# Optimization experiments

Measured on AMD Instinct MI355X. Metric: run time of the kernel, lower is better.

The kernel has to match this reference:

```python
import jax, jax.numpy as jnp
import numpy as np

SIGMA_PRIOR = 0.5   # sigma init kwarg; logvar_prior = log(sigma), sigma_prior = exp(logvar_prior) = sigma
TEMP = 1.0
LN_EPS = 1e-5
DIM, NQ, NK = 256, 512, 512


def setup_inputs() -> dict:
    key = jax.random.key(0)
    ks = jax.random.split(key, 10)
    s = 1.0 / np.sqrt(DIM)
    return {
        "Q": jax.random.normal(ks[0], (NQ, DIM), jnp.float32),
        "K": jax.random.normal(ks[1], (NK, DIM), jnp.float32),
        "V": jax.random.normal(ks[2], (NK, DIM), jnp.float32),
        "eps": jax.random.normal(ks[3], (NQ, NK), jnp.float32),
        # prior MLP: Linear(dim,dim) -> ReLU -> Linear(dim,1)
        "W1p": jax.random.normal(ks[4], (DIM, DIM), jnp.float32) * s,
        "b1p": jnp.zeros((DIM,), jnp.float32),
        "w2p": jax.random.normal(ks[5], (DIM,), jnp.float32) * s,
        "b2p": jnp.zeros((), jnp.float32),
        # posterior MLP: Linear(2*dim, dim) -> ReLU
        "Wpost": jax.random.normal(ks[6], (DIM, 2 * DIM), jnp.float32) * s,
        "bpost": jnp.zeros((DIM,), jnp.float32),
        # mu / logvar heads: Linear(dim, 1)
        "w_mu": jax.random.normal(ks[7], (DIM,), jnp.float32) * s,
        "b_mu": jnp.zeros((), jnp.float32),
        "w_lv": jax.random.normal(ks[8], (DIM,), jnp.float32) * s,
        "b_lv": jnp.zeros((), jnp.float32),
        # output LayerNorm(dim)
        "gamma": jnp.ones((DIM,), jnp.float32),
        "beta": jnp.zeros((DIM,), jnp.float32),
    }


def reference(Q, K, V, eps, W1p, b1p, w2p, b2p, Wpost, bpost,
              w_mu, b_mu, w_lv, b_lv, gamma, beta):
    dim = Q.shape[-1]
    sigma_prior = jnp.float32(SIGMA_PRIOR)

    # --- prior: mlp_prior(K) per key; broadcast over queries (identical math to K_exp) ---
    h = jax.nn.relu(K @ W1p.T + b1p)                       # [Nk, dim]
    mu_prior = h @ w2p + b2p - 0.5 * sigma_prior ** 2      # [Nk]

    # --- posterior: Linear on cat([Q_exp, K_exp]) == Q@Wq^T + K@Wk^T + b ---
    Wq, Wk = Wpost[:, :dim], Wpost[:, dim:]
    latent = jax.nn.relu((Q @ Wq.T)[:, None, :] + (K @ Wk.T + bpost)[None, :, :])  # [Nq, Nk, dim]
    phi = latent @ w_mu + b_mu                             # [Nq, Nk]
    logvar = latent @ w_lv + b_lv                          # [Nq, Nk]
    sig = jnp.exp(0.5 * logvar)
    mu = phi - 0.5 * sig ** 2

    # --- KL(prior || posterior form used by the module) ---
    term0 = jnp.log(sigma_prior / sig)
    term1 = (sig ** 2 + (mu - mu_prior[None, :]) ** 2) / (2.0 * sigma_prior ** 2)
    kl = jnp.mean(term0 + term1 - 0.5)

    # --- reparameterized sample, softmax weights, context ---
    samples = jnp.exp(mu + sig * eps) / TEMP               # [Nq, Nk]
    weights = jax.nn.softmax(samples, axis=-1)
    context = weights @ V                                  # [Nq, dim]

    # --- LayerNorm(dim) ---
    m = jnp.mean(context, axis=-1, keepdims=True)
    v = jnp.var(context, axis=-1, keepdims=True)
    out = (context - m) / jnp.sqrt(v + LN_EPS) * gamma + beta
    return (out, kl)
```

## Files before the change

kernel.cpp:

```cpp
#include <hip/hip_runtime.h>
#include <hip/hip_fp16.h>
#include <math.h>

#define DIM 256
#define NQ  512
#define NK  512

#define WS_A   0
#define WS_B   (NQ*DIM)
#define WS_MP  (WS_B + NK*DIM)
#define WS_S   (WS_MP + 512)
#define WS_P   (WS_S + NQ*NK)
#define WS_VH  (WS_P + 256)

__global__ __launch_bounds__(512) void k1_precompute(
    const float* __restrict__ Q, const float* __restrict__ Km,
    const float* __restrict__ V,
    const float* __restrict__ W1p, const float* __restrict__ b1p,
    const float* __restrict__ w2p, const float* __restrict__ b2p,
    const float* __restrict__ Wpost, const float* __restrict__ bpost,
    float* __restrict__ A, float* __restrict__ B, float* __restrict__ mu_prior,
    __half2* __restrict__ Vh2)
{
    __shared__ float X_lds[4][DIM];
    __shared__ float red[2][4][260];
    const int tid = threadIdx.x;
    const int bid = blockIdx.x;
    const int job = bid >> 7;

    if (job == 3) {
        const int pb = (bid - 384) * 4096 + tid;
        #pragma unroll
        for (int j = 0; j < 8; ++j) {
            int p = pb + 512 * j;
            float2 f = ((const float2*)V)[p];
            Vh2[p] = __floats2half2_rn(f.x, f.y);
        }
        return;
    }

    const int r0  = (bid & 127) * 4;
    const float* X = (job == 0) ? Q : Km;
    const float* W = (job == 2) ? W1p : Wpost;
    const int wstride = (job == 2) ? DIM : 2 * DIM;
    const int wcol    = (job == 1) ? DIM : 0;

    if (tid < 256) {
        int row = tid >> 6, c4 = tid & 63;
        *(float4*)&X_lds[row][c4 * 4] = *(const float4*)&X[(r0 + row) * DIM + c4 * 4];
    }
    __syncthreads();

    const int c  = tid & 255;
    const int dh = tid >> 8;
    const float* wrow = W + c * wstride + wcol + dh * 128;
    const float* xrow0 = &X_lds[0][dh * 128];

    float acc0 = 0.f, acc1 = 0.f, acc2 = 0.f, acc3 = 0.f;
    #pragma unroll 8
    for (int d0 = 0; d0 < 128; d0 += 4) {
        float4 w4 = *(const float4*)&wrow[d0];
        float4 x0 = *(const float4*)&xrow0[d0];
        float4 x1 = *(const float4*)&xrow0[DIM + d0];
        float4 x2 = *(const float4*)&xrow0[2 * DIM + d0];
        float4 x3 = *(const float4*)&xrow0[3 * DIM + d0];
        acc0 = fmaf(x0.x, w4.x, acc0); acc0 = fmaf(x0.y, w4.y, acc0);
        acc0 = fmaf(x0.z, w4.z, acc0); acc0 = fmaf(x0.w, w4.w, acc0);
        acc1 = fmaf(x1.x, w4.x, acc1); acc1 = fmaf(x1.y, w4.y, acc1);
        acc1 = fmaf(x1.z, w4.z, acc1); acc1 = fmaf(x1.w, w4.w, acc1);
        acc2 = fmaf(x2.x, w4.x, acc2); acc2 = fmaf(x2.y, w4.y, acc2);
        acc2 = fmaf(x2.z, w4.z, acc2); acc2 = fmaf(x2.w, w4.w, acc2);
        acc3 = fmaf(x3.x, w4.x, acc3); acc3 = fmaf(x3.y, w4.y, acc3);
        acc3 = fmaf(x3.z, w4.z, acc3); acc3 = fmaf(x3.w, w4.w, acc3);
    }
    red[dh][0][c] = acc0; red[dh][1][c] = acc1;
    red[dh][2][c] = acc2; red[dh][3][c] = acc3;
    __syncthreads();

    if (job < 2) {
        if (tid < 256) {
            #pragma unroll
            for (int r = 0; r < 4; ++r) {
                float v = red[0][r][c] + red[1][r][c];
                if (job == 0) A[(r0 + r) * DIM + c] = v;
                else          B[(r0 + r) * DIM + c] = v + bpost[c];
            }
        }
    } else {
        if (tid < 256) {
            float b1 = b1p[c], w2 = w2p[c];
            #pragma unroll
            for (int r = 0; r < 4; ++r)
                red[0][r][c] = fmaxf(red[0][r][c] + red[1][r][c] + b1, 0.f) * w2;
        }
        __syncthreads();
        int w = tid >> 6, lane = tid & 63;
        if (w < 4) {
            float v = red[0][w][lane] + red[0][w][lane + 64]
                    + red[0][w][lane + 128] + red[0][w][lane + 192];
            #pragma unroll
            for (int off = 32; off; off >>= 1) v += __shfl_xor(v, off);
            if (lane == 0) mu_prior[r0 + w] = v + b2p[0] - 0.125f;
        }
    }
}

__global__ __launch_bounds__(512) void k2_latent(
    const float* __restrict__ A, const float* __restrict__ B,
    const float* __restrict__ mu_prior, const float* __restrict__ eps,
    const float* __restrict__ w_mu, const float* __restrict__ b_mu,
    const float* __restrict__ w_lv, const float* __restrict__ b_lv,
    float* __restrict__ samples, float* __restrict__ partials)
{
    __shared__ float A_lds[32][260];
    __shared__ float B_lds[32][260];
    __shared__ float wm[DIM], wl[DIM];
    __shared__ float red[2][256][9];
    __shared__ float wred[8];
    const int tid = threadIdx.x;
    const int bq0 = (blockIdx.x >> 4) * 32;
    const int bk0 = (blockIdx.x & 15) * 32;

    #pragma unroll
    for (int i = 0; i < 4; ++i) {
        int f4 = tid + 512 * i;
        int row = f4 >> 6, c4 = f4 & 63;
        *(float4*)&A_lds[row][c4 * 4] = *(const float4*)&A[(bq0 + row) * DIM + c4 * 4];
        *(float4*)&B_lds[row][c4 * 4] = *(const float4*)&B[(bk0 + row) * DIM + c4 * 4];
    }
    if (tid < 256) { wm[tid] = w_mu[tid]; wl[tid] = w_lv[tid]; }
    __syncthreads();

    const int l  = tid & 255;
    const int dh = tid >> 8;
    const int tq = l >> 4, tk = l & 15;
    const int db = dh * 128;

    float p00 = 0, p01 = 0, p10 = 0, p11 = 0;
    float l00 = 0, l01 = 0, l10 = 0, l11 = 0;

    #pragma unroll 4
    for (int dd = 0; dd < 128; dd += 4) {
        int d0 = db + dd;
        float4 a0 = *(const float4*)&A_lds[tq][d0];
        float4 a1 = *(const float4*)&A_lds[tq + 16][d0];
        float4 b0 = *(const float4*)&B_lds[tk][d0];
        float4 b1 = *(const float4*)&B_lds[tk + 16][d0];
        float4 m4 = *(const float4*)&wm[d0];
        float4 v4 = *(const float4*)&wl[d0];
#define STEP(c) { float r_;                                                      \
        r_ = fmaxf(a0.c + b0.c, 0.f); p00 = fmaf(r_, m4.c, p00); l00 = fmaf(r_, v4.c, l00); \
        r_ = fmaxf(a0.c + b1.c, 0.f); p01 = fmaf(r_, m4.c, p01); l01 = fmaf(r_, v4.c, l01); \
        r_ = fmaxf(a1.c + b0.c, 0.f); p10 = fmaf(r_, m4.c, p10); l10 = fmaf(r_, v4.c, l10); \
        r_ = fmaxf(a1.c + b1.c, 0.f); p11 = fmaf(r_, m4.c, p11); l11 = fmaf(r_, v4.c, l11); }
        STEP(x) STEP(y) STEP(z) STEP(w)
#undef STEP
    }

    red[dh][l][0] = p00; red[dh][l][1] = l00;
    red[dh][l][2] = p01; red[dh][l][3] = l01;
    red[dh][l][4] = p10; red[dh][l][5] = l10;
    red[dh][l][6] = p11; red[dh][l][7] = l11;
    __syncthreads();

    float kls = 0.f;
    {
        const float bmu = b_mu[0], blv = b_lv[0];
        const int l2 = tid & 255;
        const int ih = tid >> 8;
        const int tq2 = l2 >> 4, tk2 = l2 & 15;
        const int q_  = bq0 + tq2 + 16 * ih;
        const int ka_ = bk0 + tk2, kb_ = ka_ + 16;
        const float mpa = mu_prior[ka_], mpb = mu_prior[kb_];
        const float C0 = -0.69314718056f - 0.5f;

#define FINISH(i, k, mp) {                                          \
        float pacc = red[0][l2][2*(i)]   + red[1][l2][2*(i)];       \
        float lacc = red[0][l2][2*(i)+1] + red[1][l2][2*(i)+1];     \
        float lv   = lacc + blv;                                    \
        float phi  = pacc + bmu;                                    \
        float sig  = __expf(0.5f * lv);                             \
        float sig2 = sig * sig;                                     \
        float mu   = phi - 0.5f * sig2;                             \
        float dm   = mu - (mp);                                     \
        kls += C0 - 0.5f * lv + 2.f * (sig2 + dm * dm);             \
        samples[q_ * NK + (k)] = __expf(mu + sig * eps[q_ * NK + (k)]); }

        FINISH(2 * ih,     ka_, mpa)
        FINISH(2 * ih + 1, kb_, mpb)
#undef FINISH
    }

    #pragma unroll
    for (int off = 32; off; off >>= 1) kls += __shfl_xor(kls, off);
    if ((tid & 63) == 0) wred[tid >> 6] = kls;
    __syncthreads();
    if (tid == 0) {
        float s = 0.f;
        #pragma unroll
        for (int i = 0; i < 8; ++i) s += wred[i];
        partials[blockIdx.x] = s;
    }
}

__global__ __launch_bounds__(512) void k3_output(
    const float* __restrict__ samples, const __half2* __restrict__ Vh2,
    const float* __restrict__ gamma, const float* __restrict__ beta,
    const float* __restrict__ partials, float* __restrict__ out)
{
    __shared__ float w_lds[2][NK];
    __shared__ float redbuf[16][DIM];
    __shared__ float sred[8][2], ssum[8][2], klr[8], lnred[8][2];
    const int tid = threadIdx.x;
    const int q0 = blockIdx.x * 2;
    const int wv = tid >> 6, lane = tid & 63;

    if (blockIdx.x == 0) {
        float v = (tid < 256) ? partials[tid] : 0.f;
        #pragma unroll
        for (int off = 32; off; off >>= 1) v += __shfl_xor(v, off);
        if (lane == 0) klr[wv] = v;
        __syncthreads();
        if (tid == 0) {
            float s = 0.f;
            #pragma unroll
            for (int i = 0; i < 8; ++i) s += klr[i];
            out[NQ * DIM] = s * (1.f / (float)(NQ * NK));
        }
    }

    float s0 = samples[q0 * NK + tid];
    float s1 = samples[(q0 + 1) * NK + tid];
    float m0 = s0, m1 = s1;
    #pragma unroll
    for (int off = 32; off; off >>= 1) {
        m0 = fmaxf(m0, __shfl_xor(m0, off));
        m1 = fmaxf(m1, __shfl_xor(m1, off));
    }
    if (lane == 0) { sred[wv][0] = m0; sred[wv][1] = m1; }
    __syncthreads();
    m0 = sred[0][0]; m1 = sred[0][1];
    #pragma unroll
    for (int i = 1; i < 8; ++i) {
        m0 = fmaxf(m0, sred[i][0]);
        m1 = fmaxf(m1, sred[i][1]);
    }
    float e0 = __expf(s0 - m0), e1 = __expf(s1 - m1);
    w_lds[0][tid] = e0;
    w_lds[1][tid] = e1;
    float t0 = e0, t1 = e1;
    #pragma unroll
    for (int off = 32; off; off >>= 1) {
        t0 += __shfl_xor(t0, off);
        t1 += __shfl_xor(t1, off);
    }
    if (lane == 0) { ssum[wv][0] = t0; ssum[wv][1] = t1; }
    __syncthreads();
    float sum0 = 0.f, sum1 = 0.f;
    #pragma unroll
    for (int i = 0; i < 8; ++i) { sum0 += ssum[i][0]; sum1 += ssum[i][1]; }
    const float inv0 = 1.f / sum0, inv1 = 1.f / sum1;

    const int g = tid & 63, s = tid >> 6;
    float a00 = 0, a01 = 0, a02 = 0, a03 = 0;
    float a10 = 0, a11 = 0, a12 = 0, a13 = 0;
    const __half2* vp = Vh2 + s * 64 * (DIM / 2) + 2 * g;
    #pragma unroll 8
    for (int i = 0; i < 64; ++i) {
        float2 raw = *(const float2*)(vp + i * (DIM / 2));
        __half2 h0 = *(__half2*)&raw.x;
        __half2 h1 = *(__half2*)&raw.y;
        float2 f0 = __half22float2(h0);
        float2 f1 = __half22float2(h1);
        int k = s * 64 + i;
        float w0 = w_lds[0][k], w1 = w_lds[1][k];
        a00 = fmaf(w0, f0.x, a00); a01 = fmaf(w0, f0.y, a01);
        a02 = fmaf(w0, f1.x, a02); a03 = fmaf(w0, f1.y, a03);
        a10 = fmaf(w1, f0.x, a10); a11 = fmaf(w1, f0.y, a11);
        a12 = fmaf(w1, f1.x, a12); a13 = fmaf(w1, f1.y, a13);
    }
    *(float4*)&redbuf[s * 2 + 0][4 * g] = make_float4(a00, a01, a02, a03);
    *(float4*)&redbuf[s * 2 + 1][4 * g] = make_float4(a10, a11, a12, a13);
    __syncthreads();

    const int r = tid >> 8, col = tid & 255;
    float c = 0.f;
    #pragma unroll
    for (int j = 0; j < 8; ++j) c += redbuf[j * 2 + r][col];
    c *= (r == 0) ? inv0 : inv1;
    float s1v = c, s2v = c * c;
    #pragma unroll
    for (int off = 32; off; off >>= 1) {
        s1v += __shfl_xor(s1v, off);
        s2v += __shfl_xor(s2v, off);
    }
    if (lane == 0) { lnred[wv][0] = s1v; lnred[wv][1] = s2v; }
    __syncthreads();
    float mean = (lnred[4 * r][0] + lnred[4 * r + 1][0] + lnred[4 * r + 2][0] + lnred[4 * r + 3][0]) * (1.f / DIM);
    float msq  = (lnred[4 * r][1] + lnred[4 * r + 1][1] + lnred[4 * r + 2][1] + lnred[4 * r + 3][1]) * (1.f / DIM);
    float var  = msq - mean * mean;
    out[(q0 + r) * DIM + col] = (c - mean) * rsqrtf(var + 1e-5f) * gamma[col] + beta[col];
}

extern "C" void kernel_launch(void* const* d_in, const int* in_sizes, int n_in,
                              void* d_out, int out_size, void* d_ws, size_t ws_size,
                              hipStream_t stream)
{
    (void)in_sizes; (void)n_in; (void)out_size; (void)ws_size;
    const float* Q     = (const float*)d_in[0];
    const float* K     = (const float*)d_in[1];
    const float* V     = (const float*)d_in[2];
    const float* eps   = (const float*)d_in[3];
    const float* W1p   = (const float*)d_in[4];
    const float* b1p   = (const float*)d_in[5];
    const float* w2p   = (const float*)d_in[6];
    const float* b2p   = (const float*)d_in[7];
    const float* Wpost = (const float*)d_in[8];
    const float* bpost = (const float*)d_in[9];
    const float* w_mu  = (const float*)d_in[10];
    const float* b_mu  = (const float*)d_in[11];
    const float* w_lv  = (const float*)d_in[12];
    const float* b_lv  = (const float*)d_in[13];
    const float* gamma = (const float*)d_in[14];
    const float* beta  = (const float*)d_in[15];
    float* out = (float*)d_out;
    float* wsf = (float*)d_ws;

    float*   A        = wsf + WS_A;
    float*   B        = wsf + WS_B;
    float*   mu_prior = wsf + WS_MP;
    float*   samples  = wsf + WS_S;
    float*   partials = wsf + WS_P;
    __half2* Vh2      = (__half2*)(wsf + WS_VH);

    k1_precompute<<<dim3(400), dim3(512), 0, stream>>>(
        Q, K, V, W1p, b1p, w2p, b2p, Wpost, bpost, A, B, mu_prior, Vh2);
    k2_latent<<<dim3(256), dim3(512), 0, stream>>>(
        A, B, mu_prior, eps, w_mu, b_mu, w_lv, b_lv, samples, partials);
    k3_output<<<dim3(256), dim3(512), 0, stream>>>(
        samples, Vh2, gamma, beta, partials, out);
}
```

Baseline: 123.0 us.

## Retile latent kernel with 2x4 register tiles, swizzled LDS, shuffle reduction

Restructures the latent/KL kernel so each thread computes a 2x4 (q,k) tile over a quarter of the feature dimension instead of 2x2 over half. The A/B shared tiles are XOR-swizzled to avoid bank conflicts under the new access pattern. The cross-thread reduction now uses wave shuffles rather than a shared-memory buffer and an extra barrier, and w_mu/w_lv are read from global memory instead of being staged in LDS. This raises arithmetic reuse per LDS load and cuts shared-memory traffic and sync, at the cost of more live registers per thread.

```diff
diff --git a/kernel.cpp b/kernel.cpp
--- a/kernel.cpp
+++ b/kernel.cpp
@@ -114,8 +114,6 @@
 {
     __shared__ float A_lds[32][260];
     __shared__ float B_lds[32][260];
-    __shared__ float wm[DIM], wl[DIM];
-    __shared__ float red[2][256][9];
     __shared__ float wred[8];
     const int tid = threadIdx.x;
     const int bq0 = (blockIdx.x >> 4) * 32;
@@ -125,71 +123,80 @@
     for (int i = 0; i < 4; ++i) {
         int f4 = tid + 512 * i;
         int row = f4 >> 6, c4 = f4 & 63;
-        *(float4*)&A_lds[row][c4 * 4] = *(const float4*)&A[(bq0 + row) * DIM + c4 * 4];
-        *(float4*)&B_lds[row][c4 * 4] = *(const float4*)&B[(bk0 + row) * DIM + c4 * 4];
-    }
-    if (tid < 256) { wm[tid] = w_mu[tid]; wl[tid] = w_lv[tid]; }
-    __syncthreads();
-
-    const int l  = tid & 255;
-    const int dh = tid >> 8;
-    const int tq = l >> 4, tk = l & 15;
-    const int db = dh * 128;
-
-    float p00 = 0, p01 = 0, p10 = 0, p11 = 0;
-    float l00 = 0, l01 = 0, l10 = 0, l11 = 0;
+        int pc  = (c4 & 48) | ((c4 ^ (c4 >> 4)) & 15);
+        *(float4*)&A_lds[row][pc * 4] = *(const float4*)&A[(bq0 + row) * DIM + c4 * 4];
+        *(float4*)&B_lds[row][pc * 4] = *(const float4*)&B[(bk0 + row) * DIM + c4 * 4];
+    }
+    __syncthreads();
+
+    const int tk = tid & 7;
+    const int dq = (tid >> 3) & 3;
+    const int tq = tid >> 5;
+    const int d_base = dq * 64;
+
+    float p00 = 0, p01 = 0, p02 = 0, p03 = 0;
+    float p10 = 0, p11 = 0, p12 = 0, p13 = 0;
+    float l00 = 0, l01 = 0, l02 = 0, l03 = 0;
+    float l10 = 0, l11 = 0, l12 = 0, l13 = 0;
 
     #pragma unroll 4
-    for (int dd = 0; dd < 128; dd += 4) {
-        int d0 = db + dd;
-        float4 a0 = *(const float4*)&A_lds[tq][d0];
-        float4 a1 = *(const float4*)&A_lds[tq + 16][d0];
-        float4 b0 = *(const float4*)&B_lds[tk][d0];
-        float4 b1 = *(const float4*)&B_lds[tk + 16][d0];
-        float4 m4 = *(const float4*)&wm[d0];
-        float4 v4 = *(const float4*)&wl[d0];
-#define STEP(c) { float r_;                                                      \
+    for (int dd = 0; dd < 16; ++dd) {
+        const int d0p = d_base + ((dd ^ dq) << 2);
+        const int d0w = d_base + (dd << 2);
+        float4 a0 = *(const float4*)&A_lds[tq][d0p];
+        float4 a1 = *(const float4*)&A_lds[tq + 16][d0p];
+        float4 b0 = *(const float4*)&B_lds[tk][d0p];
+        float4 b1 = *(const float4*)&B_lds[tk + 8][d0p];
+        float4 b2 = *(const float4*)&B_lds[tk + 16][d0p];
+        float4 b3 = *(const float4*)&B_lds[tk + 24][d0p];
+        float4 m4 = *(const float4*)&w_mu[d0w];
+        float4 v4 = *(const float4*)&w_lv[d0w];
+#define STEP(c) { float r_;                                                     \
         r_ = fmaxf(a0.c + b0.c, 0.f); p00 = fmaf(r_, m4.c, p00); l00 = fmaf(r_, v4.c, l00); \
         r_ = fmaxf(a0.c + b1.c, 0.f); p01 = fmaf(r_, m4.c, p01); l01 = fmaf(r_, v4.c, l01); \
+        r_ = fmaxf(a0.c + b2.c, 0.f); p02 = fmaf(r_, m4.c, p02); l02 = fmaf(r_, v4.c, l02); \
+        r_ = fmaxf(a0.c + b3.c, 0.f); p03 = fmaf(r_, m4.c, p03); l03 = fmaf(r_, v4.c, l03); \
         r_ = fmaxf(a1.c + b0.c, 0.f); p10 = fmaf(r_, m4.c, p10); l10 = fmaf(r_, v4.c, l10); \
-        r_ = fmaxf(a1.c + b1.c, 0.f); p11 = fmaf(r_, m4.c, p11); l11 = fmaf(r_, v4.c, l11); }
+        r_ = fmaxf(a1.c + b1.c, 0.f); p11 = fmaf(r_, m4.c, p11); l11 = fmaf(r_, v4.c, l11); \
+        r_ = fmaxf(a1.c + b2.c, 0.f); p12 = fmaf(r_, m4.c, p12); l12 = fmaf(r_, v4.c, l12); \
+        r_ = fmaxf(a1.c + b3.c, 0.f); p13 = fmaf(r_, m4.c, p13); l13 = fmaf(r_, v4.c, l13); }
         STEP(x) STEP(y) STEP(z) STEP(w)
 #undef STEP
     }
 
-    red[dh][l][0] = p00; red[dh][l][1] = l00;
-    red[dh][l][2] = p01; red[dh][l][3] = l01;
-    red[dh][l][4] = p10; red[dh][l][5] = l10;
-    red[dh][l][6] = p11; red[dh][l][7] = l11;
-    __syncthreads();
-
+#define RED(v) { v += __shfl_xor(v, 8); v += __shfl_xor(v, 16); }
+    RED(p00) RED(p01) RED(p02) RED(p03)
+    RED(p10) RED(p11) RED(p12) RED(p13)
+    RED(l00) RED(l01) RED(l02) RED(l03)
+    RED(l10) RED(l11) RED(l12) RED(l13)
+#undef RED
+
+    float pa, la, pb, lb;
+    if      (dq == 0) { pa = p00; la = l00; pb = p10; lb = l10; }
+    else if (dq == 1) { pa = p01; la = l01; pb = p11; lb = l11; }
+    else if (dq == 2) { pa = p02; la = l02; pb = p12; lb = l12; }
+    else              { pa = p03; la = l03; pb = p13; lb = l13; }
+
+    const int   k_own = bk0 + (tid & 31);
+    const int   qa    = bq0 + tq, qb = qa + 16;
+    const float mpk   = mu_prior[k_own];
+    const float bmu = b_mu[0], blv = b_lv[0];
+    const float C0 = -0.69314718056f - 0.5f;
     float kls = 0.f;
-    {
-        const float bmu = b_mu[0], blv = b_lv[0];
-        const int l2 = tid & 255;
-        const int ih = tid >> 8;
-        const int tq2 = l2 >> 4, tk2 = l2 & 15;
-        const int q_  = bq0 + tq2 + 16 * ih;
-        const int ka_ = bk0 + tk2, kb_ = ka_ + 16;
-        const float mpa = mu_prior[ka_], mpb = mu_prior[kb_];
-        const float C0 = -0.69314718056f - 0.5f;
-
-#define FINISH(i, k, mp) {                                          \
-        float pacc = red[0][l2][2*(i)]   + red[1][l2][2*(i)];       \
-        float lacc = red[0][l2][2*(i)+1] + red[1][l2][2*(i)+1];     \
-        float lv   = lacc + blv;                                    \
-        float phi  = pacc + bmu;                                    \
-        float sig  = __expf(0.5f * lv);                             \
+
+#define FINISH(pacc, lacc, q) {                                     \
+        float lv_  = (lacc) + blv;                                  \
+        float phi  = (pacc) + bmu;                                  \
+        float sig  = __expf(0.5f * lv_);                            \
         float sig2 = sig * sig;                                     \
         float mu   = phi - 0.5f * sig2;                             \
-        float dm   = mu - (mp);                                     \
-        kls += C0 - 0.5f * lv + 2.f * (sig2 + dm * dm);             \
-        samples[q_ * NK + (k)] = __expf(mu + sig * eps[q_ * NK + (k)]); }
-
-        FINISH(2 * ih,     ka_, mpa)
-        FINISH(2 * ih + 1, kb_, mpb)
+        float dm   = mu - mpk;                                      \
+        kls += C0 - 0.5f * lv_ + 2.f * (sig2 + dm * dm);            \
+        samples[(q) * NK + k_own] = __expf(mu + sig * eps[(q) * NK + k_own]); }
+
+    FINISH(pa, la, qa)
+    FINISH(pb, lb, qb)
 #undef FINISH
-    }
 
     #pragma unroll
     for (int off = 32; off; off >>= 1) kls += __shfl_xor(kls, off);
```

After: 124.0 us. Within noise of the previous version (+0.9%).
